# Performance work log

Hardware: AMD Instinct MI355X
Metric: run time of the kernel (lower is better)

## Reference

```python
import jax, jax.numpy as jnp
import numpy as np

ALPHA = 0.5
NEG_MASK = 1000000.0


def setup_inputs() -> dict:
    key = jax.random.key(0)
    k1, k2, k3, k4 = jax.random.split(key, 4)
    B, Dv, Nq, Ns, D = 64, 1024, 32, 1024, 128
    return {
        "q_single": jax.random.normal(k1, (B, Dv), dtype=jnp.float32),
        "d_single": jax.random.normal(k2, (B, Dv), dtype=jnp.float32),
        "q_multi": jax.random.normal(k3, (B, Nq, D), dtype=jnp.float32),
        "d_multi": jax.random.normal(k4, (B, Ns, D), dtype=jnp.float32),
    }


def _single_vector_loss(q_single, d_single):
    # scores: [B, B]
    scores = jnp.einsum('bd,cd->bc', q_single, d_single)
    # MatryoshkaCELoss iterates rows of scores; each row is CE'd against its
    # diagonal target and the per-row losses are summed (relative_importance=None -> ones).
    logp = jax.nn.log_softmax(scores, axis=-1)
    return -jnp.sum(jnp.diagonal(logp))


def _multi_vector_loss(q_multi, d_multi):
    B = q_multi.shape[0]
    # [B, B, Nq, Ns] late-interaction score tensor -> max over doc tokens, sum over query tokens
    sim = jnp.einsum('bnd,csd->bcns', q_multi, d_multi)
    scores = jnp.sum(jnp.max(sim, axis=3), axis=2)  # [B, B]
    pos_scores = jnp.diagonal(scores)
    neg_scores = jnp.max(scores - jnp.eye(B, dtype=scores.dtype) * NEG_MASK, axis=1)
    return jnp.mean(jax.nn.softplus(neg_scores - pos_scores))


def reference(q_single, d_single, q_multi, d_multi):
    sv = _single_vector_loss(q_single, d_single)
    mv = _multi_vector_loss(q_multi, d_multi)
    return ALPHA * sv + (1.0 - ALPHA) * mv
```

## Files before the change

kernel.cpp:

```cpp
#include <hip/hip_runtime.h>
#include <hip/hip_bf16.h>
#include <math.h>

#define BSZ 64
#define DV  1024
#define NQ  32
#define NS  1024
#define DD  128

#define ALPHA 0.5f

typedef __attribute__((ext_vector_type(8))) short short8;
typedef __attribute__((ext_vector_type(4))) float floatx4;

__device__ __forceinline__ unsigned short bf16_of(float x) {
    __hip_bfloat16 h = __float2bfloat16(x);
    return *(unsigned short*)&h;
}

__global__ void prep_kernel(const float* __restrict__ qm, const float* __restrict__ dm,
                            const float* __restrict__ qs, const float* __restrict__ ds,
                            unsigned short* __restrict__ qbs, unsigned short* __restrict__ dbs,
                            float* __restrict__ svrow) {
    __shared__ float row[BSZ];
    int bid = blockIdx.x, t = threadIdx.x;
    if (bid < 1024) {
#pragma unroll
        for (int it = 0; it < 4; ++it) {
            int g = it * 262144 + bid * 256 + t;
            int l = g & 63, ks = (g >> 6) & 3, st = (g >> 8) & 63, c = g >> 14;
            int srcrow = st * 16 + (l & 15);
            int kb = ks * 32 + ((l >> 4) & 3) * 8;
            const float* p = dm + ((size_t)(c * NS + srcrow)) * DD + kb;
            float4 v0 = *(const float4*)p;
            float4 v1 = *(const float4*)(p + 4);
            short8 o;
            o[0] = (short)bf16_of(v0.x); o[1] = (short)bf16_of(v0.y);
            o[2] = (short)bf16_of(v0.z); o[3] = (short)bf16_of(v0.w);
            o[4] = (short)bf16_of(v1.x); o[5] = (short)bf16_of(v1.y);
            o[6] = (short)bf16_of(v1.z); o[7] = (short)bf16_of(v1.w);
            *(short8*)(dbs + (size_t)g * 8) = o;
        }
    } else if (bid < 1056) {
#pragma unroll
        for (int it = 0; it < 4; ++it) {
            int h = it * 8192 + (bid - 1024) * 256 + t;
            int l = h & 63, ks = (h >> 6) & 3, nt = (h >> 8) & 1, b = h >> 9;
            int srcrow = b * NQ + nt * 16 + (l & 15);
            int kb = ks * 32 + ((l >> 4) & 3) * 8;
            const float* p = qm + (size_t)srcrow * DD + kb;
            float4 v0 = *(const float4*)p;
            float4 v1 = *(const float4*)(p + 4);
            short8 o;
            o[0] = (short)bf16_of(v0.x); o[1] = (short)bf16_of(v0.y);
            o[2] = (short)bf16_of(v0.z); o[3] = (short)bf16_of(v0.w);
            o[4] = (short)bf16_of(v1.x); o[5] = (short)bf16_of(v1.y);
            o[6] = (short)bf16_of(v1.z); o[7] = (short)bf16_of(v1.w);
            *(short8*)(qbs + (size_t)h * 8) = o;
        }
    } else {
        int b = bid - 1056;
        int c = t >> 2, part = t & 3;
        const float4* qv = (const float4*)(qs + b * DV);
        const float4* dv = (const float4*)(ds + c * DV);
        float acc = 0.f;
        int k0 = part * 64;
#pragma unroll 8
        for (int k = k0; k < k0 + 64; ++k) {
            float4 a = qv[k], bb = dv[k];
            acc += a.x * bb.x + a.y * bb.y + a.z * bb.z + a.w * bb.w;
        }
        acc += __shfl_xor(acc, 1);
        acc += __shfl_xor(acc, 2);
        if (part == 0) row[c] = acc;
        __syncthreads();
        if (t < BSZ) {
            float v = row[t];
            float m = v;
#pragma unroll
            for (int o = 1; o < 64; o <<= 1) m = fmaxf(m, __shfl_xor(m, o));
            float e = expf(v - m);
#pragma unroll
            for (int o = 1; o < 64; o <<= 1) e += __shfl_xor(e, o);
            float lse = m + logf(e);
            if (t == 0) svrow[b] = lse - row[b];
        }
    }
}

__launch_bounds__(256, 2)
__global__ void multi_kernel(const unsigned short* __restrict__ qbs,
                             const unsigned short* __restrict__ dbs,
                             float* __restrict__ scores) {
    int bid = blockIdx.x;
    int x = bid & 7, rr = bid >> 3;
    int c  = x * 8 + (rr & 7);
    int bg = rr >> 3;
    int t  = threadIdx.x;
    int w  = t >> 6;
    int l  = t & 63;
    int lane16 = l & 15;
    int quad   = (l >> 4) & 3;

    __shared__ float smax[4][4][NQ];

    short8 af[4][2][4];
#pragma unroll
    for (int bi = 0; bi < 4; ++bi)
#pragma unroll
        for (int nt = 0; nt < 2; ++nt)
#pragma unroll
            for (int ks = 0; ks < 4; ++ks)
                af[bi][nt][ks] = *(const short8*)(qbs +
                    ((size_t)((((bg * 4 + bi) * 2 + nt) * 4 + ks) * 64 + l)) * 8);

    float mx[4][2][4];
#pragma unroll
    for (int bi = 0; bi < 4; ++bi)
#pragma unroll
        for (int nt = 0; nt < 2; ++nt)
#pragma unroll
            for (int r = 0; r < 4; ++r) mx[bi][nt][r] = -1e30f;

    short8 bf[2][4];
    auto loadb = [&](short8* dst, int st) {
        const unsigned short* p = dbs + ((size_t)((c * 64 + st) * 4) * 64 + l) * 8;
#pragma unroll
        for (int ks = 0; ks < 4; ++ks)
            dst[ks] = *(const short8*)(p + (size_t)ks * 512);
    };

    loadb(bf[0], w);
#pragma unroll
    for (int i = 0; i < 16; ++i) {
        if (i < 15) loadb(bf[(i + 1) & 1], w + (i + 1) * 4);
        const short8* B = bf[i & 1];
        floatx4 acc[4][2];
#pragma unroll
        for (int bi = 0; bi < 4; ++bi)
#pragma unroll
            for (int nt = 0; nt < 2; ++nt) acc[bi][nt] = (floatx4){0.f, 0.f, 0.f, 0.f};
#pragma unroll
        for (int ks = 0; ks < 4; ++ks)
#pragma unroll
            for (int bi = 0; bi < 4; ++bi)
#pragma unroll
                for (int nt = 0; nt < 2; ++nt)
                    acc[bi][nt] = __builtin_amdgcn_mfma_f32_16x16x32_bf16(
                        af[bi][nt][ks], B[ks], acc[bi][nt], 0, 0, 0);
#pragma unroll
        for (int bi = 0; bi < 4; ++bi)
#pragma unroll
            for (int nt = 0; nt < 2; ++nt)
#pragma unroll
                for (int r = 0; r < 4; ++r)
                    mx[bi][nt][r] = fmaxf(mx[bi][nt][r], acc[bi][nt][r]);
    }

#pragma unroll
    for (int bi = 0; bi < 4; ++bi)
#pragma unroll
        for (int nt = 0; nt < 2; ++nt)
#pragma unroll
            for (int r = 0; r < 4; ++r) {
                float v = mx[bi][nt][r];
                v = fmaxf(v, __shfl_xor(v, 1));
                v = fmaxf(v, __shfl_xor(v, 2));
                v = fmaxf(v, __shfl_xor(v, 4));
                v = fmaxf(v, __shfl_xor(v, 8));
                mx[bi][nt][r] = v;
            }
    if (lane16 == 0) {
#pragma unroll
        for (int bi = 0; bi < 4; ++bi)
#pragma unroll
            for (int nt = 0; nt < 2; ++nt)
#pragma unroll
                for (int r = 0; r < 4; ++r)
                    smax[w][bi][nt * 16 + quad * 4 + r] = mx[bi][nt][r];
    }
    __syncthreads();
    if (t < 4 * NQ) {
        int bi = t >> 5, n = t & 31;
        float v = fmaxf(fmaxf(smax[0][bi][n], smax[1][bi][n]),
                        fmaxf(smax[2][bi][n], smax[3][bi][n]));
#pragma unroll
        for (int o = 1; o < 32; o <<= 1) v += __shfl_xor(v, o);
        if (n == 0) scores[(bg * 4 + bi) * BSZ + c] = v;
    }
}

__global__ void finish_kernel(const float* __restrict__ scores, const float* __restrict__ svrow,
                              float* __restrict__ out) {
    int t = threadIdx.x;
    float pos = scores[t * BSZ + t];
    float neg = -1e30f;
    for (int cc = 0; cc < BSZ; ++cc)
        if (cc != t) neg = fmaxf(neg, scores[t * BSZ + cc]);
    float xx = neg - pos;
    float sp = fmaxf(xx, 0.f) + log1pf(expf(-fabsf(xx)));
    float sv = svrow[t];
#pragma unroll
    for (int o = 1; o < 64; o <<= 1) {
        sp += __shfl_xor(sp, o);
        sv += __shfl_xor(sv, o);
    }
    if (t == 0) out[0] = ALPHA * sv + (1.0f - ALPHA) * (sp * (1.0f / BSZ));
}

extern "C" void kernel_launch(void* const* d_in, const int* in_sizes, int n_in,
                              void* d_out, int out_size, void* d_ws, size_t ws_size,
                              hipStream_t stream) {
    const float* q_single = (const float*)d_in[0];
    const float* d_single = (const float*)d_in[1];
    const float* q_multi  = (const float*)d_in[2];
    const float* d_multi  = (const float*)d_in[3];
    float* out = (float*)d_out;

    unsigned short* qbs = (unsigned short*)d_ws;
    unsigned short* dbs = (unsigned short*)((char*)d_ws + 524288);
    float* scores       = (float*)((char*)d_ws + 524288 + 16777216);
    float* svrow        = (float*)((char*)d_ws + 524288 + 16777216 + 16384);

    prep_kernel<<<1120, 256, 0, stream>>>(q_multi, d_multi, q_single, d_single,
                                          qbs, dbs, svrow);
    multi_kernel<<<1024, 256, 0, stream>>>(qbs, dbs, scores);
    finish_kernel<<<1, 64, 0, stream>>>(scores, svrow, out);
}
```

Baseline: 138.3 us.

## Switch multi-vector similarity from bf16 MFMA to scaled fp8 MFMA

The multi-vector inputs are now converted to fp8 (packed via cvt_pk_fp8) in a re-tiled layout instead of bf16. The late-interaction matmul uses the scaled 16x16x128 f8f6f4 MFMA, so one instruction covers the whole 128-wide K dimension. This halves the intermediate buffer traffic and the MFMA count, and the prep kernel launches fewer blocks. The cost is lower precision in the max-sim scores, which may move the loss beyond tolerance.

```diff
diff --git a/kernel.cpp b/kernel.cpp
--- a/kernel.cpp
+++ b/kernel.cpp
@@ -10,56 +10,51 @@
 
 #define ALPHA 0.5f
 
-typedef __attribute__((ext_vector_type(8))) short short8;
+typedef __attribute__((ext_vector_type(8))) int   int8v;
 typedef __attribute__((ext_vector_type(4))) float floatx4;
-
-__device__ __forceinline__ unsigned short bf16_of(float x) {
-    __hip_bfloat16 h = __float2bfloat16(x);
-    return *(unsigned short*)&h;
-}
+#define SCALE1 127
 
 __global__ void prep_kernel(const float* __restrict__ qm, const float* __restrict__ dm,
                             const float* __restrict__ qs, const float* __restrict__ ds,
-                            unsigned short* __restrict__ qbs, unsigned short* __restrict__ dbs,
+                            unsigned char* __restrict__ qb8, unsigned char* __restrict__ db8,
                             float* __restrict__ svrow) {
     __shared__ float row[BSZ];
     int bid = blockIdx.x, t = threadIdx.x;
-    if (bid < 1024) {
+    int w = t >> 6, l = t & 63;
+    int lane16 = l & 15, quad = (l >> 4) & 3;
+
+    auto cvt_chunk = [&](const float* src, unsigned char* dst) {
+        int dw[8];
+#pragma unroll
+        for (int j = 0; j < 8; ++j) {
+            float4 v = ((const float4*)src)[j];
+            int d0 = __builtin_amdgcn_cvt_pk_fp8_f32(v.x, v.y, 0, false);
+            dw[j]  = __builtin_amdgcn_cvt_pk_fp8_f32(v.z, v.w, d0, true);
+        }
+        ((int4*)dst)[0] = make_int4(dw[0], dw[1], dw[2], dw[3]);
+        ((int4*)dst)[1] = make_int4(dw[4], dw[5], dw[6], dw[7]);
+    };
+
+    if (bid < 256) {
+        int gw = bid * 4 + w;
 #pragma unroll
         for (int it = 0; it < 4; ++it) {
-            int g = it * 262144 + bid * 256 + t;
-            int l = g & 63, ks = (g >> 6) & 3, st = (g >> 8) & 63, c = g >> 14;
-            int srcrow = st * 16 + (l & 15);
-            int kb = ks * 32 + ((l >> 4) & 3) * 8;
-            const float* p = dm + ((size_t)(c * NS + srcrow)) * DD + kb;
-            float4 v0 = *(const float4*)p;
-            float4 v1 = *(const float4*)(p + 4);
-            short8 o;
-            o[0] = (short)bf16_of(v0.x); o[1] = (short)bf16_of(v0.y);
-            o[2] = (short)bf16_of(v0.z); o[3] = (short)bf16_of(v0.w);
-            o[4] = (short)bf16_of(v1.x); o[5] = (short)bf16_of(v1.y);
-            o[6] = (short)bf16_of(v1.z); o[7] = (short)bf16_of(v1.w);
-            *(short8*)(dbs + (size_t)g * 8) = o;
-        }
-    } else if (bid < 1056) {
+            int ch = gw + it * 1024;
+            int c = ch >> 6, st = ch & 63;
+            const float* src = dm + ((size_t)(c * NS + st * 16 + lane16)) * DD + quad * 32;
+            cvt_chunk(src, db8 + (size_t)ch * 2048 + l * 32);
+        }
+    } else if (bid < 264) {
+        int gw = (bid - 256) * 4 + w;
 #pragma unroll
         for (int it = 0; it < 4; ++it) {
-            int h = it * 8192 + (bid - 1024) * 256 + t;
-            int l = h & 63, ks = (h >> 6) & 3, nt = (h >> 8) & 1, b = h >> 9;
-            int srcrow = b * NQ + nt * 16 + (l & 15);
-            int kb = ks * 32 + ((l >> 4) & 3) * 8;
-            const float* p = qm + (size_t)srcrow * DD + kb;
-            float4 v0 = *(const float4*)p;
-            float4 v1 = *(const float4*)(p + 4);
-            short8 o;
-            o[0] = (short)bf16_of(v0.x); o[1] = (short)bf16_of(v0.y);
-            o[2] = (short)bf16_of(v0.z); o[3] = (short)bf16_of(v0.w);
-            o[4] = (short)bf16_of(v1.x); o[5] = (short)bf16_of(v1.y);
-            o[6] = (short)bf16_of(v1.z); o[7] = (short)bf16_of(v1.w);
-            *(short8*)(qbs + (size_t)h * 8) = o;
+            int ch = gw * 4 + it;
+            int b = ch >> 1, nt = ch & 1;
+            const float* src = qm + ((size_t)(b * NQ + nt * 16 + lane16)) * DD + quad * 32;
+            cvt_chunk(src, qb8 + (size_t)ch * 2048 + l * 32);
         }
     } else {
-        int b = bid - 1056;
+        int b = bid - 264;
         int c = t >> 2, part = t & 3;
         const float4* qv = (const float4*)(qs + b * DV);
         const float4* dv = (const float4*)(ds + c * DV);
@@ -89,8 +84,8 @@
 }
 
 __launch_bounds__(256, 2)
-__global__ void multi_kernel(const unsigned short* __restrict__ qbs,
-                             const unsigned short* __restrict__ dbs,
+__global__ void multi_kernel(const unsigned char* __restrict__ qb8,
+                             const unsigned char* __restrict__ db8,
                              float* __restrict__ scores) {
     int bid = blockIdx.x;
     int x = bid & 7, rr = bid >> 3;
@@ -104,15 +99,13 @@
 
     __shared__ float smax[4][4][NQ];
 
-    short8 af[4][2][4];
+    int8v af[4][2];
 #pragma unroll
     for (int bi = 0; bi < 4; ++bi)
 #pragma unroll
         for (int nt = 0; nt < 2; ++nt)
-#pragma unroll
-            for (int ks = 0; ks < 4; ++ks)
-                af[bi][nt][ks] = *(const short8*)(qbs +
-                    ((size_t)((((bg * 4 + bi) * 2 + nt) * 4 + ks) * 64 + l)) * 8);
+            af[bi][nt] = *(const int8v*)(qb8 +
+                (size_t)(((bg * 4 + bi) * 2 + nt) * 2048) + l * 32);
 
     float mx[4][2][4];
 #pragma unroll
@@ -122,39 +115,29 @@
 #pragma unroll
             for (int r = 0; r < 4; ++r) mx[bi][nt][r] = -1e30f;
 
-    short8 bf[2][4];
-    auto loadb = [&](short8* dst, int st) {
-        const unsigned short* p = dbs + ((size_t)((c * 64 + st) * 4) * 64 + l) * 8;
-#pragma unroll
-        for (int ks = 0; ks < 4; ++ks)
-            dst[ks] = *(const short8*)(p + (size_t)ks * 512);
+    int8v bf[2];
+    auto loadb = [&](int which, int st) {
+        bf[which] = *(const int8v*)(db8 + (size_t)((c * 64 + st) * 2048) + l * 32);
     };
 
-    loadb(bf[0], w);
+    loadb(0, w);
 #pragma unroll
     for (int i = 0; i < 16; ++i) {
-        if (i < 15) loadb(bf[(i + 1) & 1], w + (i + 1) * 4);
-        const short8* B = bf[i & 1];
-        floatx4 acc[4][2];
+        if (i < 15) loadb((i + 1) & 1, w + (i + 1) * 4);
+        int8v B = bf[i & 1];
 #pragma unroll
         for (int bi = 0; bi < 4; ++bi)
 #pragma unroll
-            for (int nt = 0; nt < 2; ++nt) acc[bi][nt] = (floatx4){0.f, 0.f, 0.f, 0.f};
-#pragma unroll
-        for (int ks = 0; ks < 4; ++ks)
-#pragma unroll
-            for (int bi = 0; bi < 4; ++bi)
-#pragma unroll
-                for (int nt = 0; nt < 2; ++nt)
-                    acc[bi][nt] = __builtin_amdgcn_mfma_f32_16x16x32_bf16(
-                        af[bi][nt][ks], B[ks], acc[bi][nt], 0, 0, 0);
-#pragma unroll
-        for (int bi = 0; bi < 4; ++bi)
-#pragma unroll
-            for (int nt = 0; nt < 2; ++nt)
+            for (int nt = 0; nt < 2; ++nt) {
+                floatx4 acc = __builtin_amdgcn_mfma_scale_f32_16x16x128_f8f6f4(
+                    af[bi][nt], B, (floatx4){0.f, 0.f, 0.f, 0.f},
+                    0, 0,
+                    0, SCALE1,
+                    0, SCALE1);
 #pragma unroll
                 for (int r = 0; r < 4; ++r)
-                    mx[bi][nt][r] = fmaxf(mx[bi][nt][r], acc[bi][nt][r]);
+                    mx[bi][nt][r] = fmaxf(mx[bi][nt][r], acc[r]);
+            }
     }
 
 #pragma unroll
@@ -217,13 +200,13 @@
     const float* d_multi  = (const float*)d_in[3];
     float* out = (float*)d_out;
 
-    unsigned short* qbs = (unsigned short*)d_ws;
-    unsigned short* dbs = (unsigned short*)((char*)d_ws + 524288);
-    float* scores       = (float*)((char*)d_ws + 524288 + 16777216);
-    float* svrow        = (float*)((char*)d_ws + 524288 + 16777216 + 16384);
-
-    prep_kernel<<<1120, 256, 0, stream>>>(q_multi, d_multi, q_single, d_single,
-                                          qbs, dbs, svrow);
-    multi_kernel<<<1024, 256, 0, stream>>>(qbs, dbs, scores);
+    unsigned char* qb8 = (unsigned char*)d_ws;
+    unsigned char* db8 = (unsigned char*)d_ws + 262144;
+    float* scores      = (float*)((char*)d_ws + 262144 + 8388608);
+    float* svrow       = (float*)((char*)d_ws + 262144 + 8388608 + 16384);
+
+    prep_kernel<<<328, 256, 0, stream>>>(q_multi, d_multi, q_single, d_single,
+                                         qb8, db8, svrow);
+    multi_kernel<<<1024, 256, 0, stream>>>(qb8, db8, scores);
     finish_kernel<<<1, 64, 0, stream>>>(scores, svrow, out);
 }
```

Measured after the change: 122.9 us. 11.1% less time.
